# Performance work log

Measured on AMD Instinct MI355X. Metric: run time of the kernel, lower is better.

## Reference

```python
import jax, jax.numpy as jnp
import numpy as np

D = 1024
H = 16
HD = D // H
SCALE = HD ** -0.5


def setup_inputs() -> dict:
    key = jax.random.key(0)
    ks = jax.random.split(key, 5)
    x = jax.random.normal(ks[0], (2, 2048, D), dtype=jnp.float32)
    s = 1.0 / np.sqrt(D)
    W_qkv = jax.random.uniform(ks[1], (D, 3 * D), jnp.float32, -s, s)
    b_qkv = jax.random.uniform(ks[2], (3 * D,), jnp.float32, -s, s)
    W_out = jax.random.uniform(ks[3], (D, D), jnp.float32, -s, s)
    b_out = jax.random.uniform(ks[4], (D,), jnp.float32, -s, s)
    return {"x": x, "W_qkv": W_qkv, "b_qkv": b_qkv, "W_out": W_out, "b_out": b_out}


def reference(x, W_qkv, b_qkv, W_out, b_out):
    B, S, _ = x.shape
    qkv = x @ W_qkv + b_qkv                       # [B,S,3D]
    qkv = qkv.reshape(B, S, 3, H, HD)
    q, k, v = jnp.moveaxis(qkv, 2, 0)             # each [B,S,H,HD]
    # scores: [B,H,S,S]
    scores = jnp.einsum("bshd,bthd->bhst", q, k) * SCALE
    attn = jax.nn.softmax(scores, axis=-1)        # dropout is identity in eval mode
    out = jnp.einsum("bhst,bthd->bshd", attn, v)  # [B,S,H,HD]
    out = out.reshape(B, S, H * HD)
    return out @ W_out + b_out
```

## Files before the change

### kernel.cpp

```cpp
#include <hip/hip_runtime.h>

typedef unsigned short u16;
typedef unsigned int   u32;

using short8 = __attribute__((ext_vector_type(8))) short;
using f32x4  = __attribute__((ext_vector_type(4))) float;
using half4  = __attribute__((ext_vector_type(4))) _Float16;

#define QSCALE 0.18033688011112042f

__device__ __forceinline__ u16 f2bf(float f) {
  u32 u = __float_as_uint(f);
  return (u16)((u + 0x8000u) >> 16);
}
__device__ __forceinline__ u16 f2h(float f) {
  _Float16 h = (_Float16)f;
  return __builtin_bit_cast(u16, h);
}

__device__ __forceinline__ void gld16(const u16* g, u16* l) {
  __builtin_amdgcn_global_load_lds(
      (const __attribute__((address_space(1))) unsigned int*)g,
      (__attribute__((address_space(3))) unsigned int*)l, 16, 0, 0);
}

__global__ __launch_bounds__(256) void cvt_x(const float* __restrict__ in,
                                             u16* __restrict__ out) {
  int idx = blockIdx.x * 256 + threadIdx.x;
  float4 v = reinterpret_cast<const float4*>(in)[idx];
  ushort4 o;
  o.x = f2bf(v.x); o.y = f2bf(v.y); o.z = f2bf(v.z); o.w = f2bf(v.w);
  reinterpret_cast<ushort4*>(out)[idx] = o;
}

__global__ __launch_bounds__(256) void transpose_w(const float* __restrict__ in,
                                                   u16* __restrict__ out,
                                                   int R, int C) {
  __shared__ u32 s[32][33];
  int c0 = blockIdx.x * 32, r0 = blockIdx.y * 32;
  int j = threadIdx.x & 31, i0 = threadIdx.x >> 5;
#pragma unroll
  for (int p = 0; p < 4; ++p) {
    int i = i0 + p * 8;
    s[i][j] = f2bf(in[(size_t)(r0 + i) * C + c0 + j]);
  }
  __syncthreads();
#pragma unroll
  for (int p = 0; p < 4; ++p) {
    int jj = i0 + p * 8;
    out[(size_t)(c0 + jj) * R + r0 + j] = (u16)s[j][jj];
  }
}

template <int EPI, int MT>
__global__ __launch_bounds__(256, 3) void gemm_bt(
    const u16* __restrict__ A, const u16* __restrict__ Bt,
    const float* __restrict__ bias, float* __restrict__ c_out,
    u16* __restrict__ q_out, u16* __restrict__ k_out, u16* __restrict__ vt_out,
    int M, int N, int K) {
  __shared__ __align__(16) u16 As[32 * MT * 32];
  __shared__ __align__(16) u16 Bs[128 * 32];
  const int tid = threadIdx.x;
  const int lane = tid & 63;
  const int wv = tid >> 6;
  const int l16 = lane & 15, quad = lane >> 4;
  const int wm = wv & 1, wn = wv >> 1;
  const int bx = blockIdx.x, by = blockIdx.y;

  const u16* Ab = A + (size_t)by * (32 * MT) * K;
  const u16* Bb = Bt + (size_t)bx * 128 * K;

  const f32x4 fzero = {0.0f, 0.0f, 0.0f, 0.0f};
  f32x4 acc[MT][4];
#pragma unroll
  for (int i = 0; i < MT; ++i)
#pragma unroll
    for (int j = 0; j < 4; ++j) acc[i][j] = fzero;

  for (int k0 = 0; k0 < K; k0 += 32) {
    __syncthreads();
#pragma unroll
    for (int p = 0; p < MT / 2; ++p) {
      int id = p * 256 + tid;
      int row = id >> 2, blk = id & 3;
      int gc = k0 + ((blk ^ (row & 3)) << 3);
      gld16(Ab + (size_t)row * K + gc, &As[id << 3]);
    }
#pragma unroll
    for (int p = 0; p < 2; ++p) {
      int id = p * 256 + tid;
      int row = id >> 2, blk = id & 3;
      int gc = k0 + ((blk ^ (row & 3)) << 3);
      gld16(Bb + (size_t)row * K + gc, &Bs[id << 3]);
    }
    __syncthreads();
    short8 af[MT], bfr[4];
#pragma unroll
    for (int mi = 0; mi < MT; ++mi) {
      int row = wm * (MT * 16) + mi * 16 + l16;
      af[mi] = *reinterpret_cast<const short8*>(&As[row * 32 + ((quad ^ (row & 3)) << 3)]);
    }
#pragma unroll
    for (int ni = 0; ni < 4; ++ni) {
      int row = wn * 64 + ni * 16 + l16;
      bfr[ni] = *reinterpret_cast<const short8*>(&Bs[row * 32 + ((quad ^ (row & 3)) << 3)]);
    }
#pragma unroll
    for (int mi = 0; mi < MT; ++mi)
#pragma unroll
      for (int ni = 0; ni < 4; ++ni)
        acc[mi][ni] = __builtin_amdgcn_mfma_f32_16x16x32_bf16(af[mi], bfr[ni], acc[mi][ni], 0, 0, 0);
  }

#pragma unroll
  for (int mi = 0; mi < MT; ++mi)
#pragma unroll
    for (int ni = 0; ni < 4; ++ni) {
      int col = bx * 128 + wn * 64 + ni * 16 + l16;
      float bv = bias[col];
      int row0 = by * (32 * MT) + wm * (MT * 16) + mi * 16 + quad * 4;
      if (EPI == 1) {
#pragma unroll
        for (int r = 0; r < 4; ++r)
          c_out[(size_t)(row0 + r) * N + col] = acc[mi][ni][r] + bv;
      } else {
        int which = col >> 10, rem = col & 1023;
        int h = rem >> 6, d = rem & 63;
        int b = row0 >> 11, sq0 = row0 & 2047;
        int bh = (b << 4) + h;
        if (which == 2) {
          int tile = sq0 >> 6;
          int sub = ((sq0 >> 2) & 15) ^ (d & 15);
          ushort4 pk;
          pk.x = f2h(acc[mi][ni][0] + bv);
          pk.y = f2h(acc[mi][ni][1] + bv);
          pk.z = f2h(acc[mi][ni][2] + bv);
          pk.w = f2h(acc[mi][ni][3] + bv);
          *reinterpret_cast<ushort4*>(
              &vt_out[(size_t)bh * 131072 + tile * 4096 + d * 64 + (sub << 2)]) = pk;
        } else {
          size_t base = (size_t)(bh * 2048 + sq0) * 64 + d;
#pragma unroll
          for (int r = 0; r < 4; ++r) {
            float val = acc[mi][ni][r] + bv;
            if (which == 0) q_out[base + r * 64] = f2bf(val * QSCALE);
            else            k_out[base + r * 64] = f2bf(val);
          }
        }
      }
    }
}

__global__ __launch_bounds__(256, 5) void attn(
    const u16* __restrict__ q_buf, const u16* __restrict__ k_buf,
    const u16* __restrict__ vt_buf, u16* __restrict__ o_buf) {
  __shared__ __align__(16) u16 smem[2][2][4096];

  const int tid = threadIdx.x;
  const int lane = tid & 63, w = tid >> 6;
  const int l16 = lane & 15, quad = lane >> 4;
  const int bh = blockIdx.y, q0 = blockIdx.x * 32;

  const u16* qg = q_buf + (size_t)bh * 131072 + q0 * 64;
  const u16* kg = k_buf + (size_t)bh * 131072;
  const u16* vg = vt_buf + (size_t)bh * 131072;

  short8 qb[2][2];
#pragma unroll
  for (int qi = 0; qi < 2; ++qi)
#pragma unroll
    for (int kk = 0; kk < 2; ++kk)
      qb[qi][kk] = *reinterpret_cast<const short8*>(
          qg + (qi * 16 + l16) * 64 + kk * 32 + quad * 8);

#pragma unroll
  for (int p = 0; p < 2; ++p) {
    int id = p * 256 + tid;
    int row = id >> 3, blk = id & 7;
    gld16(kg + row * 64 + ((blk ^ (row & 7)) << 3), &smem[0][0][id << 3]);
    gld16(vg + id * 8, &smem[0][1][id << 3]);
  }

  const f32x4 fzero = {0.0f, 0.0f, 0.0f, 0.0f};
  f32x4 o_acc[2][4];
  float l_acc[2] = {0.f, 0.f};
#pragma unroll
  for (int qi = 0; qi < 2; ++qi)
#pragma unroll
    for (int nd = 0; nd < 4; ++nd) o_acc[qi][nd] = fzero;

  const int kr = w * 16 + l16;
  const int ka_off0 = kr * 64 + ((quad ^ (kr & 7)) << 3);
  const int ka_off1 = kr * 64 + (((4 + quad) ^ (kr & 7)) << 3);
  const int vb_off = l16 * 64 + (((w * 4 + quad) ^ l16) << 2);

  __syncthreads();

  for (int i = 0; i < 32; ++i) {
    const int buf = i & 1;
    if (i + 1 < 32) {
      const int nxt = buf ^ 1;
#pragma unroll
      for (int p = 0; p < 2; ++p) {
        int id = p * 256 + tid;
        int row = id >> 3, blk = id & 7;
        gld16(kg + ((i + 1) * 64 + row) * 64 + ((blk ^ (row & 7)) << 3),
              &smem[nxt][0][id << 3]);
        gld16(vg + (i + 1) * 4096 + id * 8, &smem[nxt][1][id << 3]);
      }
    }

    short8 ka0 = *reinterpret_cast<const short8*>(&smem[buf][0][ka_off0]);
    short8 ka1 = *reinterpret_cast<const short8*>(&smem[buf][0][ka_off1]);
    f32x4 s[2];
#pragma unroll
    for (int qi = 0; qi < 2; ++qi) {
      s[qi] = __builtin_amdgcn_mfma_f32_16x16x32_bf16(ka0, qb[qi][0], fzero, 0, 0, 0);
      s[qi] = __builtin_amdgcn_mfma_f32_16x16x32_bf16(ka1, qb[qi][1], s[qi], 0, 0, 0);
    }

    half4 pa[2];
#pragma unroll
    for (int qi = 0; qi < 2; ++qi) {
      float p0 = __builtin_amdgcn_exp2f(s[qi][0]);
      float p1 = __builtin_amdgcn_exp2f(s[qi][1]);
      float p2 = __builtin_amdgcn_exp2f(s[qi][2]);
      float p3 = __builtin_amdgcn_exp2f(s[qi][3]);
      l_acc[qi] += (p0 + p1) + (p2 + p3);
      pa[qi][0] = (_Float16)p0; pa[qi][1] = (_Float16)p1;
      pa[qi][2] = (_Float16)p2; pa[qi][3] = (_Float16)p3;
    }

#pragma unroll
    for (int nd = 0; nd < 4; ++nd) {
      half4 vb = *reinterpret_cast<const half4*>(&smem[buf][1][vb_off + nd * 1024]);
#pragma unroll
      for (int qi = 0; qi < 2; ++qi)
        o_acc[qi][nd] = __builtin_amdgcn_mfma_f32_16x16x16f16(pa[qi], vb, o_acc[qi][nd], 0, 0, 0);
    }

    __syncthreads();
  }

#pragma unroll
  for (int qi = 0; qi < 2; ++qi) {
    l_acc[qi] += __shfl_xor(l_acc[qi], 16, 64);
    l_acc[qi] += __shfl_xor(l_acc[qi], 32, 64);
  }

  float* fb = (float*)smem;
  const int b = bh >> 4, h = bh & 15;
#pragma unroll
  for (int qi = 0; qi < 2; ++qi) {
#pragma unroll
    for (int nd = 0; nd < 4; ++nd)
      *reinterpret_cast<f32x4*>(&fb[((w * 4 + nd) * 64 + lane) * 4]) = o_acc[qi][nd];
    if (lane < 16) fb[4096 + w * 16 + lane] = l_acc[qi];
    __syncthreads();
    f32x4 os = fzero, lv = fzero;
#pragma unroll
    for (int wp = 0; wp < 4; ++wp) {
      os += *reinterpret_cast<const f32x4*>(&fb[((wp * 4 + w) * 64 + lane) * 4]);
      lv += *reinterpret_cast<const f32x4*>(&fb[4096 + wp * 16 + quad * 4]);
    }
#pragma unroll
    for (int r = 0; r < 4; ++r) {
      int sq = q0 + qi * 16 + quad * 4 + r;
      o_buf[(size_t)(b * 2048 + sq) * 1024 + h * 64 + w * 16 + l16] =
          f2bf(os[r] / lv[r]);
    }
    __syncthreads();
  }
}

extern "C" void kernel_launch(void* const* d_in, const int* in_sizes, int n_in,
                              void* d_out, int out_size, void* d_ws, size_t ws_size,
                              hipStream_t stream) {
  (void)in_sizes; (void)n_in; (void)out_size; (void)ws_size;
  const float* x     = (const float*)d_in[0];
  const float* W_qkv = (const float*)d_in[1];
  const float* b_qkv = (const float*)d_in[2];
  const float* W_out = (const float*)d_in[3];
  const float* b_out = (const float*)d_in[4];
  float* out = (float*)d_out;

  char* ws = (char*)d_ws;
  u16* x_bf   = (u16*)(ws);
  u16* wqkv_t = (u16*)(ws + 8388608);
  u16* wout_t = (u16*)(ws + 14680064);
  u16* q_buf  = (u16*)(ws + 16777216);
  u16* k_buf  = (u16*)(ws + 25165824);
  u16* vt_buf = (u16*)(ws + 33554432);
  u16* o_bf   = (u16*)(ws + 41943040);

  cvt_x<<<4096, 256, 0, stream>>>(x, x_bf);
  transpose_w<<<dim3(96, 32), 256, 0, stream>>>(W_qkv, wqkv_t, 1024, 3072);
  transpose_w<<<dim3(32, 32), 256, 0, stream>>>(W_out, wout_t, 1024, 1024);
  gemm_bt<0, 4><<<dim3(24, 32), 256, 0, stream>>>(x_bf, wqkv_t, b_qkv, nullptr,
                                                  q_buf, k_buf, vt_buf, 4096, 3072, 1024);
  attn<<<dim3(64, 32), 256, 0, stream>>>(q_buf, k_buf, vt_buf, o_bf);
  gemm_bt<1, 2><<<dim3(8, 64), 256, 0, stream>>>(o_bf, wout_t, b_out, out,
                                                 nullptr, nullptr, nullptr, 4096, 1024, 1024);
}
```

Baseline: 196.8 us.

## Load K/V fragments directly to registers in attention, drop LDS staging

```diff
diff --git a/kernel.cpp b/kernel.cpp
--- a/kernel.cpp
+++ b/kernel.cpp
@@ -6,6 +6,7 @@
 using short8 = __attribute__((ext_vector_type(8))) short;
 using f32x4  = __attribute__((ext_vector_type(4))) float;
 using half4  = __attribute__((ext_vector_type(4))) _Float16;
+using half8  = __attribute__((ext_vector_type(8))) _Float16;
 
 #define QSCALE 0.18033688011112042f
 
@@ -129,15 +130,14 @@
         int b = row0 >> 11, sq0 = row0 & 2047;
         int bh = (b << 4) + h;
         if (which == 2) {
-          int tile = sq0 >> 6;
-          int sub = ((sq0 >> 2) & 15) ^ (d & 15);
           ushort4 pk;
           pk.x = f2h(acc[mi][ni][0] + bv);
           pk.y = f2h(acc[mi][ni][1] + bv);
           pk.z = f2h(acc[mi][ni][2] + bv);
           pk.w = f2h(acc[mi][ni][3] + bv);
-          *reinterpret_cast<ushort4*>(
-              &vt_out[(size_t)bh * 131072 + tile * 4096 + d * 64 + (sub << 2)]) = pk;
+          size_t off = (size_t)bh * 131072 +
+                       (((sq0 >> 2) * 16 + (d & 15)) * 16 + ((d >> 4) << 2));
+          *reinterpret_cast<ushort4*>(&vt_out[off]) = pk;
         } else {
           size_t base = (size_t)(bh * 2048 + sq0) * 64 + d;
 #pragma unroll
@@ -151,117 +151,104 @@
     }
 }
 
-__global__ __launch_bounds__(256, 5) void attn(
+__global__ __launch_bounds__(256, 3) void attn(
     const u16* __restrict__ q_buf, const u16* __restrict__ k_buf,
     const u16* __restrict__ vt_buf, u16* __restrict__ o_buf) {
-  __shared__ __align__(16) u16 smem[2][2][4096];
+  __shared__ __align__(16) float red[4][4][256];
+  __shared__ float lred[4][16];
 
   const int tid = threadIdx.x;
   const int lane = tid & 63, w = tid >> 6;
   const int l16 = lane & 15, quad = lane >> 4;
-  const int bh = blockIdx.y, q0 = blockIdx.x * 32;
+  const int bh = blockIdx.x, q0 = blockIdx.y * 64;
 
   const u16* qg = q_buf + (size_t)bh * 131072 + q0 * 64;
-  const u16* kg = k_buf + (size_t)bh * 131072;
-  const u16* vg = vt_buf + (size_t)bh * 131072;
-
-  short8 qb[2][2];
-#pragma unroll
-  for (int qi = 0; qi < 2; ++qi)
+  const u16* kp = k_buf + (size_t)bh * 131072 + (w * 16 + l16) * 64 + quad * 8;
+  const u16* vp = vt_buf + (size_t)bh * 131072 + ((w * 4 + quad) * 16 + l16) * 16;
+
+  short8 qb[4][2];
+#pragma unroll
+  for (int qi = 0; qi < 4; ++qi)
 #pragma unroll
     for (int kk = 0; kk < 2; ++kk)
       qb[qi][kk] = *reinterpret_cast<const short8*>(
           qg + (qi * 16 + l16) * 64 + kk * 32 + quad * 8);
 
-#pragma unroll
-  for (int p = 0; p < 2; ++p) {
-    int id = p * 256 + tid;
-    int row = id >> 3, blk = id & 7;
-    gld16(kg + row * 64 + ((blk ^ (row & 7)) << 3), &smem[0][0][id << 3]);
-    gld16(vg + id * 8, &smem[0][1][id << 3]);
-  }
-
   const f32x4 fzero = {0.0f, 0.0f, 0.0f, 0.0f};
-  f32x4 o_acc[2][4];
-  float l_acc[2] = {0.f, 0.f};
-#pragma unroll
-  for (int qi = 0; qi < 2; ++qi)
+  f32x4 o_acc[4][4];
+  float l_acc[4] = {0.f, 0.f, 0.f, 0.f};
+#pragma unroll
+  for (int qi = 0; qi < 4; ++qi)
 #pragma unroll
     for (int nd = 0; nd < 4; ++nd) o_acc[qi][nd] = fzero;
 
-  const int kr = w * 16 + l16;
-  const int ka_off0 = kr * 64 + ((quad ^ (kr & 7)) << 3);
-  const int ka_off1 = kr * 64 + (((4 + quad) ^ (kr & 7)) << 3);
-  const int vb_off = l16 * 64 + (((w * 4 + quad) ^ l16) << 2);
-
-  __syncthreads();
-
+  short8 ka[2][2];
+  half8  vf[2][2];
+  ka[0][0] = *reinterpret_cast<const short8*>(kp);
+  ka[0][1] = *reinterpret_cast<const short8*>(kp + 32);
+  vf[0][0] = *reinterpret_cast<const half8*>(vp);
+  vf[0][1] = *reinterpret_cast<const half8*>(vp + 8);
+
+#pragma unroll 2
   for (int i = 0; i < 32; ++i) {
-    const int buf = i & 1;
+    const int buf = i & 1, nb = buf ^ 1;
     if (i + 1 < 32) {
-      const int nxt = buf ^ 1;
-#pragma unroll
-      for (int p = 0; p < 2; ++p) {
-        int id = p * 256 + tid;
-        int row = id >> 3, blk = id & 7;
-        gld16(kg + ((i + 1) * 64 + row) * 64 + ((blk ^ (row & 7)) << 3),
-              &smem[nxt][0][id << 3]);
-        gld16(vg + (i + 1) * 4096 + id * 8, &smem[nxt][1][id << 3]);
-      }
-    }
-
-    short8 ka0 = *reinterpret_cast<const short8*>(&smem[buf][0][ka_off0]);
-    short8 ka1 = *reinterpret_cast<const short8*>(&smem[buf][0][ka_off1]);
-    f32x4 s[2];
-#pragma unroll
-    for (int qi = 0; qi < 2; ++qi) {
-      s[qi] = __builtin_amdgcn_mfma_f32_16x16x32_bf16(ka0, qb[qi][0], fzero, 0, 0, 0);
-      s[qi] = __builtin_amdgcn_mfma_f32_16x16x32_bf16(ka1, qb[qi][1], s[qi], 0, 0, 0);
-    }
-
-    half4 pa[2];
-#pragma unroll
-    for (int qi = 0; qi < 2; ++qi) {
-      float p0 = __builtin_amdgcn_exp2f(s[qi][0]);
-      float p1 = __builtin_amdgcn_exp2f(s[qi][1]);
-      float p2 = __builtin_amdgcn_exp2f(s[qi][2]);
-      float p3 = __builtin_amdgcn_exp2f(s[qi][3]);
+      const u16* kn = kp + (size_t)4096;
+      const u16* vn = vp + (size_t)4096;
+      ka[nb][0] = *reinterpret_cast<const short8*>(kn);
+      ka[nb][1] = *reinterpret_cast<const short8*>(kn + 32);
+      vf[nb][0] = *reinterpret_cast<const half8*>(vn);
+      vf[nb][1] = *reinterpret_cast<const half8*>(vn + 8);
+      kp = kn; vp = vn;
+    }
+
+    short8 k0 = ka[buf][0], k1 = ka[buf][1];
+    half4 pa[4];
+#pragma unroll
+    for (int qi = 0; qi < 4; ++qi) {
+      f32x4 s = __builtin_amdgcn_mfma_f32_16x16x32_bf16(k0, qb[qi][0], fzero, 0, 0, 0);
+      s = __builtin_amdgcn_mfma_f32_16x16x32_bf16(k1, qb[qi][1], s, 0, 0, 0);
+      float p0 = __builtin_amdgcn_exp2f(s[0]);
+      float p1 = __builtin_amdgcn_exp2f(s[1]);
+      float p2 = __builtin_amdgcn_exp2f(s[2]);
+      float p3 = __builtin_amdgcn_exp2f(s[3]);
       l_acc[qi] += (p0 + p1) + (p2 + p3);
       pa[qi][0] = (_Float16)p0; pa[qi][1] = (_Float16)p1;
       pa[qi][2] = (_Float16)p2; pa[qi][3] = (_Float16)p3;
     }
 
-#pragma unroll
-    for (int nd = 0; nd < 4; ++nd) {
-      half4 vb = *reinterpret_cast<const half4*>(&smem[buf][1][vb_off + nd * 1024]);
-#pragma unroll
-      for (int qi = 0; qi < 2; ++qi)
-        o_acc[qi][nd] = __builtin_amdgcn_mfma_f32_16x16x16f16(pa[qi], vb, o_acc[qi][nd], 0, 0, 0);
-    }
-
-    __syncthreads();
-  }
-
-#pragma unroll
-  for (int qi = 0; qi < 2; ++qi) {
+    half4 vb0 = __builtin_shufflevector(vf[buf][0], vf[buf][0], 0, 1, 2, 3);
+    half4 vb1 = __builtin_shufflevector(vf[buf][0], vf[buf][0], 4, 5, 6, 7);
+    half4 vb2 = __builtin_shufflevector(vf[buf][1], vf[buf][1], 0, 1, 2, 3);
+    half4 vb3 = __builtin_shufflevector(vf[buf][1], vf[buf][1], 4, 5, 6, 7);
+#pragma unroll
+    for (int qi = 0; qi < 4; ++qi) {
+      o_acc[qi][0] = __builtin_amdgcn_mfma_f32_16x16x16f16(pa[qi], vb0, o_acc[qi][0], 0, 0, 0);
+      o_acc[qi][1] = __builtin_amdgcn_mfma_f32_16x16x16f16(pa[qi], vb1, o_acc[qi][1], 0, 0, 0);
+      o_acc[qi][2] = __builtin_amdgcn_mfma_f32_16x16x16f16(pa[qi], vb2, o_acc[qi][2], 0, 0, 0);
+      o_acc[qi][3] = __builtin_amdgcn_mfma_f32_16x16x16f16(pa[qi], vb3, o_acc[qi][3], 0, 0, 0);
+    }
+  }
+
+#pragma unroll
+  for (int qi = 0; qi < 4; ++qi) {
     l_acc[qi] += __shfl_xor(l_acc[qi], 16, 64);
     l_acc[qi] += __shfl_xor(l_acc[qi], 32, 64);
   }
 
-  float* fb = (float*)smem;
   const int b = bh >> 4, h = bh & 15;
 #pragma unroll
-  for (int qi = 0; qi < 2; ++qi) {
+  for (int qi = 0; qi < 4; ++qi) {
 #pragma unroll
     for (int nd = 0; nd < 4; ++nd)
-      *reinterpret_cast<f32x4*>(&fb[((w * 4 + nd) * 64 + lane) * 4]) = o_acc[qi][nd];
-    if (lane < 16) fb[4096 + w * 16 + lane] = l_acc[qi];
+      *reinterpret_cast<f32x4*>(&red[w][nd][lane * 4]) = o_acc[qi][nd];
+    if (lane < 16) lred[w][lane] = l_acc[qi];
     __syncthreads();
     f32x4 os = fzero, lv = fzero;
 #pragma unroll
     for (int wp = 0; wp < 4; ++wp) {
-      os += *reinterpret_cast<const f32x4*>(&fb[((wp * 4 + w) * 64 + lane) * 4]);
-      lv += *reinterpret_cast<const f32x4*>(&fb[4096 + wp * 16 + quad * 4]);
+      os += *reinterpret_cast<const f32x4*>(&red[wp][w][lane * 4]);
+      lv += *reinterpret_cast<const f32x4*>(&lred[wp][quad * 4]);
     }
 #pragma unroll
     for (int r = 0; r < 4; ++r) {
@@ -298,7 +285,7 @@
   transpose_w<<<dim3(32, 32), 256, 0, stream>>>(W_out, wout_t, 1024, 1024);
   gemm_bt<0, 4><<<dim3(24, 32), 256, 0, stream>>>(x_bf, wqkv_t, b_qkv, nullptr,
                                                   q_buf, k_buf, vt_buf, 4096, 3072, 1024);
-  attn<<<dim3(64, 32), 256, 0, stream>>>(q_buf, k_buf, vt_buf, o_bf);
+  attn<<<dim3(32, 32), 256, 0, stream>>>(q_buf, k_buf, vt_buf, o_bf);
   gemm_bt<1, 2><<<dim3(8, 64), 256, 0, stream>>>(o_bf, wout_t, b_out, out,
                                                  nullptr, nullptr, nullptr, 4096, 1024, 1024);
 }
```

Result: faster. 188.9 us (-4.0%).
